# Optimization experiments

Hardware: AMD Instinct MI355X
Metric: run time of the kernel (lower is better)

## Reference

```python
import jax, jax.numpy as jnp
import numpy as np

EPS = 1e-05


def _project_to_poincare_ball(v, eps=EPS):
    # scale = clamp((1-eps)/(||v||+1e-10), max=1.0)
    norm = jnp.sqrt(jnp.sum(v * v, axis=-1, keepdims=True))
    scale = jnp.minimum((1.0 - eps) / (norm + 1e-10), 1.0)
    return v * scale


def setup_inputs() -> dict:
    key = jax.random.key(0)
    k1, k2 = jax.random.split(key)
    B, S, D, V = 2, 2048, 1024, 32000
    hidden_states = jax.random.normal(k1, (B, S, D), dtype=jnp.float32)
    weight = jax.random.normal(k2, (V, D), dtype=jnp.float32)
    return {"hidden_states": hidden_states, "weight": weight}


def reference(hidden_states, weight):
    eps = EPS
    B, S, D = hidden_states.shape
    x = _project_to_poincare_ball(hidden_states.reshape(-1, D), eps)  # (N, D)
    y = _project_to_poincare_ball(weight, eps)                        # (V, D)

    x_sq = jnp.sum(x * x, axis=-1)  # (N,)
    y_sq = jnp.sum(y * y, axis=-1)  # (V,)

    # NOTE: the original feeds this (non-squared) distance into the Poincare
    # formula (variable misnamed diff_norm_sq); we reproduce that exactly.
    d2 = x_sq[:, None] + y_sq[None, :] - 2.0 * jnp.einsum('nd,vd->nv', x, y)
    dist_euclid = jnp.sqrt(jnp.maximum(d2, 0.0))  # (N, V)

    denom = (1.0 - x_sq)[:, None] * (1.0 - y_sq)[None, :]  # (N, V)
    argument = 1.0 + 2.0 * dist_euclid / (denom + eps)
    argument = jnp.maximum(argument, 1.0 + eps)
    distances = jnp.arccosh(argument)  # (N, V)

    logits = -distances
    return logits.reshape(B, S, -1)
```

## Files before the change

### kernel.cpp

```cpp
#include <hip/hip_runtime.h>
#include <math.h>
#include <stdint.h>

#define EPS 1e-5f

typedef __bf16 bf16x8 __attribute__((ext_vector_type(8)));
typedef __bf16 bf16x4 __attribute__((ext_vector_type(4)));
typedef float  f32x4  __attribute__((ext_vector_type(4)));

constexpr int D  = 1024;

__global__ __launch_bounds__(256) void project_convert_kernel(
    const float* __restrict__ src, __bf16* __restrict__ dst,
    float* __restrict__ q_out)
{
    const int row = blockIdx.x;
    const int t = threadIdx.x;
    const float4 v = *(const float4*)(src + (size_t)row * D + t * 4);
    float s = v.x * v.x + v.y * v.y + v.z * v.z + v.w * v.w;
#pragma unroll
    for (int off = 32; off > 0; off >>= 1) s += __shfl_down(s, off);
    __shared__ float partial[4];
    __shared__ float s_scale;
    if ((t & 63) == 0) partial[t >> 6] = s;
    __syncthreads();
    if (t == 0) {
        float tot = partial[0] + partial[1] + partial[2] + partial[3];
        float norm = sqrtf(tot);
        float sc = fminf((1.0f - EPS) / (norm + 1e-10f), 1.0f);
        s_scale = sc;
        q_out[row] = sc * sc * tot;
    }
    __syncthreads();
    const float sc = s_scale;
    bf16x4 o = { (__bf16)(v.x * sc), (__bf16)(v.y * sc),
                 (__bf16)(v.z * sc), (__bf16)(v.w * sc) };
    *(bf16x4*)(dst + (size_t)row * D + t * 4) = o;
}

__device__ __forceinline__ void gload16(const void* g, void* l)
{
    __builtin_amdgcn_global_load_lds(
        (const __attribute__((address_space(1))) uint32_t*)g,
        (__attribute__((address_space(3))) uint32_t*)l, 16, 0, 0);
}

#define WAITVM(N) asm volatile("s_waitcnt vmcnt(" #N ")" ::: "memory")
#define WAITLGKM0 asm volatile("s_waitcnt lgkmcnt(0)" ::: "memory")

__global__ __launch_bounds__(512, 2) void hyp_gemm_256_kernel(
    const __bf16* __restrict__ Xb, const __bf16* __restrict__ Yb,
    const float* __restrict__ xq, const float* __restrict__ yq,
    float* __restrict__ out, int V, int nbx)
{
    constexpr int BK = 64;
    constexpr int KT = D / BK;
    constexpr int BUFB = 256 * BK * 2;

    __shared__ __bf16 As[2 * 256 * BK];
    __shared__ __bf16 Bs[2 * 256 * BK];

    const int wg = blockIdx.x;
    const int c = (gridDim.x & 7) ? wg : ((wg & 7) * (gridDim.x >> 3) + (wg >> 3));
    const int m0 = (c / nbx) * 256;
    const int n0 = (c % nbx) * 256;

    const int t = threadIdx.x;

    const int rt = t >> 3;
    const int gsrc = (t & 7) ^ (rt & 7);
    const char* xg = (const char*)(Xb + (size_t)(m0 + rt) * D) + gsrc * 16;
    const char* yg = (const char*)(Yb + (size_t)(n0 + rt) * D) + gsrc * 16;

    const int lane = t & 63;
    const int ln   = lane & 15;
    const int quad = lane >> 4;
    const int wave = t >> 6;
    const int wm = (wave >> 2) * 128;
    const int wn = (wave & 3) * 64;
    const int swz = ln & 7;

    f32x4 acc[8][4] = {};

    auto STAGE = [&](int kt, int b) {
        const int ko = kt * 128;
#pragma unroll
        for (int j = 0; j < 4; ++j)
            gload16(xg + j * 131072 + ko, (char*)As + b * BUFB + j * 8192 + t * 16);
#pragma unroll
        for (int j = 0; j < 4; ++j)
            gload16(yg + j * 131072 + ko, (char*)Bs + b * BUFB + j * 8192 + t * 16);
    };

    auto COMPUTE = [&](int b) {
        const char* Ab = (const char*)As + b * BUFB;
        const char* Bb = (const char*)Bs + b * BUFB;
#pragma unroll
        for (int ks = 0; ks < 2; ++ks) {
            const int ga = ((ks * 4 + quad) ^ swz) * 16;
            bf16x8 af[8], bfr[4];
#pragma unroll
            for (int i = 0; i < 8; ++i)
                af[i] = *(const bf16x8*)(Ab + (wm + i * 16 + ln) * 128 + ga);
#pragma unroll
            for (int i = 0; i < 4; ++i)
                bfr[i] = *(const bf16x8*)(Bb + (wn + i * 16 + ln) * 128 + ga);
            __builtin_amdgcn_s_setprio(1);
#pragma unroll
            for (int mt = 0; mt < 8; ++mt)
#pragma unroll
                for (int nt = 0; nt < 4; ++nt)
                    acc[mt][nt] = __builtin_amdgcn_mfma_f32_16x16x32_bf16(
                        af[mt], bfr[nt], acc[mt][nt], 0, 0, 0);
            __builtin_amdgcn_s_setprio(0);
        }
    };

    STAGE(0, 0);
#pragma unroll 2
    for (int kt = 0; kt < KT; ++kt) {
        const int b = kt & 1;
        if (kt + 1 < KT) {
            STAGE(kt + 1, b ^ 1);
            WAITVM(8);
        } else {
            WAITVM(0);
        }
        __builtin_amdgcn_sched_barrier(0);
        __builtin_amdgcn_s_barrier();
        __builtin_amdgcn_sched_barrier(0);
        COMPUTE(b);
        WAITLGKM0;
        __builtin_amdgcn_sched_barrier(0);
        __builtin_amdgcn_s_barrier();
        __builtin_amdgcn_sched_barrier(0);
    }

    float yqv[4], omy[4];
    int gcv[4];
#pragma unroll
    for (int nt = 0; nt < 4; ++nt) {
        const int gc = n0 + wn + nt * 16 + ln;
        gcv[nt] = gc;
        yqv[nt] = yq[gc];
        omy[nt] = 1.0f - yqv[nt];
    }
#pragma unroll
    for (int mt = 0; mt < 8; ++mt) {
#pragma unroll
        for (int r = 0; r < 4; ++r) {
            const int gm = m0 + wm + mt * 16 + quad * 4 + r;
            const float xqv = xq[gm];
            const float omx = 1.0f - xqv;
            float* orow = out + (size_t)gm * V;
#pragma unroll
            for (int nt = 0; nt < 4; ++nt) {
                const float dot = acc[mt][nt][r];
                float d2 = fmaxf(xqv + yqv[nt] - 2.0f * dot, 0.0f);
                float d  = __builtin_amdgcn_sqrtf(d2);
                float denom = omx * omy[nt] + EPS;
                float w = d * __builtin_amdgcn_rcpf(denom);
                float res;
                if (__builtin_expect(w >= 4.0f, 1)) {
                    res = __logf(2.0f + 4.0f * w);
                } else {
                    float arg = fmaxf(1.0f + 2.0f * w, 1.0f + EPS);
                    res = __logf(arg + __builtin_amdgcn_sqrtf(arg * arg - 1.0f));
                }
                orow[gcv[nt]] = -res;
            }
        }
    }
}

constexpr int FBM = 128, FBN = 128;
constexpr int LDT = 40;

__global__ __launch_bounds__(256) void row_stats_kernel(
    const float* __restrict__ src, float* __restrict__ scale_out,
    float* __restrict__ sq_out)
{
    const int row = blockIdx.x;
    const int t = threadIdx.x;
    const float4 v = *(const float4*)(src + (size_t)row * D + t * 4);
    float s = v.x * v.x + v.y * v.y + v.z * v.z + v.w * v.w;
#pragma unroll
    for (int off = 32; off > 0; off >>= 1) s += __shfl_down(s, off);
    __shared__ float partial[4];
    if ((t & 63) == 0) partial[t >> 6] = s;
    __syncthreads();
    if (t == 0) {
        float tot = partial[0] + partial[1] + partial[2] + partial[3];
        float norm = sqrtf(tot);
        float sc = fminf((1.0f - EPS) / (norm + 1e-10f), 1.0f);
        scale_out[row] = sc;
        sq_out[row] = sc * sc * tot;
    }
}

__global__ __launch_bounds__(256) void hyp_gemm_kernel(
    const float* __restrict__ X, const float* __restrict__ Y,
    const float* __restrict__ sx, const float* __restrict__ xq,
    const float* __restrict__ sy, const float* __restrict__ yq,
    float* __restrict__ out, int V)
{
    constexpr int BK = 32;
    __shared__ __bf16 As[FBM * LDT];
    __shared__ __bf16 Bs[FBN * LDT];

    const int t  = threadIdx.x;
    const int m0 = blockIdx.y * FBM;
    const int n0 = blockIdx.x * FBN;

    const int sr = t >> 3;
    const int scol = t & 7;

    const float* xg = X + (size_t)(m0 + sr) * D + scol * 4;
    const float* yg = Y + (size_t)(n0 + sr) * D + scol * 4;

    const int lane = t & 63;
    const int wave = t >> 6;
    const int wm = (wave & 1) * 64;
    const int wn = (wave >> 1) * 64;
    const int ln = lane & 15;
    const int quad = lane >> 4;

    f32x4 acc[4][4] = {};

    float4 pa[4], pb[4];
#pragma unroll
    for (int j = 0; j < 4; ++j) {
        pa[j] = *(const float4*)(xg + (size_t)j * 32 * D);
        pb[j] = *(const float4*)(yg + (size_t)j * 32 * D);
    }

    constexpr int KT = D / BK;
    for (int kt = 0; kt < KT; ++kt) {
        __syncthreads();
#pragma unroll
        for (int j = 0; j < 4; ++j) {
            bf16x4 a4 = { (__bf16)pa[j].x, (__bf16)pa[j].y, (__bf16)pa[j].z, (__bf16)pa[j].w };
            bf16x4 b4 = { (__bf16)pb[j].x, (__bf16)pb[j].y, (__bf16)pb[j].z, (__bf16)pb[j].w };
            *(bf16x4*)&As[(sr + 32 * j) * LDT + scol * 4] = a4;
            *(bf16x4*)&Bs[(sr + 32 * j) * LDT + scol * 4] = b4;
        }
        __syncthreads();
        if (kt + 1 < KT) {
            const int koff = (kt + 1) * BK;
#pragma unroll
            for (int j = 0; j < 4; ++j) {
                pa[j] = *(const float4*)(xg + (size_t)j * 32 * D + koff);
                pb[j] = *(const float4*)(yg + (size_t)j * 32 * D + koff);
            }
        }
        bf16x8 af[4], bfr[4];
#pragma unroll
        for (int i = 0; i < 4; ++i) {
            af[i]  = *(const bf16x8*)&As[(wm + i * 16 + ln) * LDT + quad * 8];
            bfr[i] = *(const bf16x8*)&Bs[(wn + i * 16 + ln) * LDT + quad * 8];
        }
#pragma unroll
        for (int mt = 0; mt < 4; ++mt)
#pragma unroll
            for (int nt = 0; nt < 4; ++nt)
                acc[mt][nt] = __builtin_amdgcn_mfma_f32_16x16x32_bf16(
                    af[mt], bfr[nt], acc[mt][nt], 0, 0, 0);
    }

    float yqv[4], syv[4];
    int gcv[4];
#pragma unroll
    for (int nt = 0; nt < 4; ++nt) {
        const int gc = n0 + wn + nt * 16 + ln;
        gcv[nt] = gc;
        yqv[nt] = yq[gc];
        syv[nt] = sy[gc];
    }
#pragma unroll
    for (int mt = 0; mt < 4; ++mt) {
#pragma unroll
        for (int r = 0; r < 4; ++r) {
            const int gm = m0 + wm + mt * 16 + quad * 4 + r;
            const float xqv = xq[gm];
            const float sxv = sx[gm];
            const float omx = 1.0f - xqv;
            float* orow = out + (size_t)gm * V;
#pragma unroll
            for (int nt = 0; nt < 4; ++nt) {
                const float raw = acc[mt][nt][r];
                const float dot = sxv * syv[nt] * raw;
                float d2 = xqv + yqv[nt] - 2.0f * dot;
                float dd = __builtin_amdgcn_sqrtf(fmaxf(d2, 0.0f));
                float denom = omx * (1.0f - yqv[nt]) + EPS;
                float arg = 1.0f + 2.0f * dd * __builtin_amdgcn_rcpf(denom);
                arg = fmaxf(arg, 1.0f + EPS);
                float res = -__logf(arg + __builtin_amdgcn_sqrtf(arg * arg - 1.0f));
                orow[gcv[nt]] = res;
            }
        }
    }
}

extern "C" void kernel_launch(void* const* d_in, const int* in_sizes, int n_in,
                              void* d_out, int out_size, void* d_ws, size_t ws_size,
                              hipStream_t stream)
{
    const float* X = (const float*)d_in[0];
    const float* Y = (const float*)d_in[1];
    float* out = (float*)d_out;

    const int N = in_sizes[0] / D;
    const int V = in_sizes[1] / D;

    const size_t need = (size_t)(N + V) * D * 2 + (size_t)(N + V) * 4;

    if (ws_size >= need && (N % 256) == 0 && (V % 256) == 0) {
        __bf16* Xb = (__bf16*)d_ws;
        __bf16* Yb = Xb + (size_t)N * D;
        float* xq = (float*)(Yb + (size_t)V * D);
        float* yq = xq + N;

        project_convert_kernel<<<N, 256, 0, stream>>>(X, Xb, xq);
        project_convert_kernel<<<V, 256, 0, stream>>>(Y, Yb, yq);

        const int nbx = V / 256;
        const int nwg = nbx * (N / 256);
        hyp_gemm_256_kernel<<<nwg, 512, 0, stream>>>(Xb, Yb, xq, yq, out, V, nbx);
    } else {
        float* sx = (float*)d_ws;
        float* xq = sx + N;
        float* sy = xq + N;
        float* yq = sy + V;

        row_stats_kernel<<<N, 256, 0, stream>>>(X, sx, xq);
        row_stats_kernel<<<V, 256, 0, stream>>>(Y, sy, yq);

        dim3 grid(V / FBN, N / FBM);
        hyp_gemm_kernel<<<grid, 256, 0, stream>>>(X, Y, sx, xq, sy, yq, out, V);
    }
}
```

Before: 909.2 us.

## Switch GEMM main loop to 4-stage BK=32 LDS ring with one barrier

Halves the K tile to 32 and uses a four-buffer LDS ring with prefetch distance two, so each iteration needs only one workgroup barrier instead of two and no explicit LDS-read wait. The XOR swizzle is reworked for the 64-byte row pitch. The goal is to overlap global-to-LDS loads with MFMA work and cut barrier stalls. In exchange there are twice as many loop iterations, smaller MFMA bursts per barrier, and possible LDS bank conflicts from the narrower swizzle.

```diff
diff --git a/kernel.cpp b/kernel.cpp
--- a/kernel.cpp
+++ b/kernel.cpp
@@ -46,19 +46,18 @@
 }
 
 #define WAITVM(N) asm volatile("s_waitcnt vmcnt(" #N ")" ::: "memory")
-#define WAITLGKM0 asm volatile("s_waitcnt lgkmcnt(0)" ::: "memory")
 
 __global__ __launch_bounds__(512, 2) void hyp_gemm_256_kernel(
     const __bf16* __restrict__ Xb, const __bf16* __restrict__ Yb,
     const float* __restrict__ xq, const float* __restrict__ yq,
     float* __restrict__ out, int V, int nbx)
 {
-    constexpr int BK = 64;
-    constexpr int KT = D / BK;
+    constexpr int BK   = 32;
+    constexpr int KT   = D / BK;
     constexpr int BUFB = 256 * BK * 2;
 
-    __shared__ __bf16 As[2 * 256 * BK];
-    __shared__ __bf16 Bs[2 * 256 * BK];
+    __shared__ __bf16 As[4 * 256 * BK];
+    __shared__ __bf16 Bs[4 * 256 * BK];
 
     const int wg = blockIdx.x;
     const int c = (gridDim.x & 7) ? wg : ((wg & 7) * (gridDim.x >> 3) + (wg >> 3));
@@ -67,8 +66,8 @@
 
     const int t = threadIdx.x;
 
-    const int rt = t >> 3;
-    const int gsrc = (t & 7) ^ (rt & 7);
+    const int rt   = t >> 2;
+    const int gsrc = (t & 3) ^ ((t >> 3) & 3);
     const char* xg = (const char*)(Xb + (size_t)(m0 + rt) * D) + gsrc * 16;
     const char* yg = (const char*)(Yb + (size_t)(n0 + rt) * D) + gsrc * 16;
 
@@ -78,63 +77,60 @@
     const int wave = t >> 6;
     const int wm = (wave >> 2) * 128;
     const int wn = (wave & 3) * 64;
-    const int swz = ln & 7;
+    const int ga = (quad ^ ((ln >> 1) & 3)) * 16;
 
     f32x4 acc[8][4] = {};
 
     auto STAGE = [&](int kt, int b) {
-        const int ko = kt * 128;
-#pragma unroll
-        for (int j = 0; j < 4; ++j)
-            gload16(xg + j * 131072 + ko, (char*)As + b * BUFB + j * 8192 + t * 16);
-#pragma unroll
-        for (int j = 0; j < 4; ++j)
-            gload16(yg + j * 131072 + ko, (char*)Bs + b * BUFB + j * 8192 + t * 16);
+        const int ko = kt * 64;
+        gload16(xg + ko,          (char*)As + b * BUFB + t * 16);
+        gload16(xg + ko + 262144, (char*)As + b * BUFB + 8192 + t * 16);
+        gload16(yg + ko,          (char*)Bs + b * BUFB + t * 16);
+        gload16(yg + ko + 262144, (char*)Bs + b * BUFB + 8192 + t * 16);
     };
 
     auto COMPUTE = [&](int b) {
         const char* Ab = (const char*)As + b * BUFB;
         const char* Bb = (const char*)Bs + b * BUFB;
-#pragma unroll
-        for (int ks = 0; ks < 2; ++ks) {
-            const int ga = ((ks * 4 + quad) ^ swz) * 16;
-            bf16x8 af[8], bfr[4];
-#pragma unroll
-            for (int i = 0; i < 8; ++i)
-                af[i] = *(const bf16x8*)(Ab + (wm + i * 16 + ln) * 128 + ga);
-#pragma unroll
-            for (int i = 0; i < 4; ++i)
-                bfr[i] = *(const bf16x8*)(Bb + (wn + i * 16 + ln) * 128 + ga);
-            __builtin_amdgcn_s_setprio(1);
-#pragma unroll
-            for (int mt = 0; mt < 8; ++mt)
-#pragma unroll
-                for (int nt = 0; nt < 4; ++nt)
-                    acc[mt][nt] = __builtin_amdgcn_mfma_f32_16x16x32_bf16(
-                        af[mt], bfr[nt], acc[mt][nt], 0, 0, 0);
-            __builtin_amdgcn_s_setprio(0);
-        }
+        bf16x8 af[8], bfr[4];
+#pragma unroll
+        for (int i = 0; i < 8; ++i)
+            af[i] = *(const bf16x8*)(Ab + (wm + i * 16 + ln) * 64 + ga);
+#pragma unroll
+        for (int i = 0; i < 4; ++i)
+            bfr[i] = *(const bf16x8*)(Bb + (wn + i * 16 + ln) * 64 + ga);
+        __builtin_amdgcn_s_setprio(1);
+#pragma unroll
+        for (int mt = 0; mt < 8; ++mt)
+#pragma unroll
+            for (int nt = 0; nt < 4; ++nt)
+                acc[mt][nt] = __builtin_amdgcn_mfma_f32_16x16x32_bf16(
+                    af[mt], bfr[nt], acc[mt][nt], 0, 0, 0);
+        __builtin_amdgcn_s_setprio(0);
     };
 
     STAGE(0, 0);
-#pragma unroll 2
-    for (int kt = 0; kt < KT; ++kt) {
-        const int b = kt & 1;
-        if (kt + 1 < KT) {
-            STAGE(kt + 1, b ^ 1);
-            WAITVM(8);
-        } else {
-            WAITVM(0);
-        }
+    STAGE(1, 1);
+
+#pragma unroll
+    for (int kt = 0; kt < KT - 2; ++kt) {
+        STAGE(kt + 2, (kt + 2) & 3);
         __builtin_amdgcn_sched_barrier(0);
+        WAITVM(8);
         __builtin_amdgcn_s_barrier();
         __builtin_amdgcn_sched_barrier(0);
-        COMPUTE(b);
-        WAITLGKM0;
-        __builtin_amdgcn_sched_barrier(0);
-        __builtin_amdgcn_s_barrier();
-        __builtin_amdgcn_sched_barrier(0);
-    }
+        COMPUTE(kt & 3);
+    }
+    __builtin_amdgcn_sched_barrier(0);
+    WAITVM(4);
+    __builtin_amdgcn_s_barrier();
+    __builtin_amdgcn_sched_barrier(0);
+    COMPUTE((KT - 2) & 3);
+    __builtin_amdgcn_sched_barrier(0);
+    WAITVM(0);
+    __builtin_amdgcn_s_barrier();
+    __builtin_amdgcn_sched_barrier(0);
+    COMPUTE((KT - 1) & 3);
 
     float yqv[4], omy[4];
     int gcv[4];
```

After: 899.4 us. About the same (-1.1%).

## Split GEMM mainloop into half-tile stages interleaved with MFMA quadrants

Applied to the files above, without the earlier changes.

Restructures the bf16 GEMM main loop so the 256x64 A/B tiles are staged as separate 128-row halves. Global-to-LDS loads for the next iterations are spread between four MFMA quadrant phases, with extra barriers, instead of one bulk prefetch per iteration. The aim is finer overlap of memory traffic with matrix compute, in the style of HipKittens 8-wave ping-pong schedules. It also drops the XCD-aware block remapping and adds many more s_barrier calls, which may add sync overhead or hurt L2 locality.

```diff
diff --git a/kernel.cpp b/kernel.cpp
--- a/kernel.cpp
+++ b/kernel.cpp
@@ -45,95 +45,156 @@
         (__attribute__((address_space(3))) uint32_t*)l, 16, 0, 0);
 }
 
-#define WAITVM(N) asm volatile("s_waitcnt vmcnt(" #N ")" ::: "memory")
-#define WAITLGKM0 asm volatile("s_waitcnt lgkmcnt(0)" ::: "memory")
+#define WAITVM(N)  asm volatile("s_waitcnt vmcnt(" #N ")" ::: "memory")
+#define WAITLGKM0  asm volatile("s_waitcnt lgkmcnt(0)" ::: "memory")
+#define SBAR()     __builtin_amdgcn_s_barrier()
+#define SCHED0()   __builtin_amdgcn_sched_barrier(0)
 
 __global__ __launch_bounds__(512, 2) void hyp_gemm_256_kernel(
     const __bf16* __restrict__ Xb, const __bf16* __restrict__ Yb,
     const float* __restrict__ xq, const float* __restrict__ yq,
     float* __restrict__ out, int V, int nbx)
 {
-    constexpr int BK = 64;
-    constexpr int KT = D / BK;
-    constexpr int BUFB = 256 * BK * 2;
-
-    __shared__ __bf16 As[2 * 256 * BK];
-    __shared__ __bf16 Bs[2 * 256 * BK];
-
-    const int wg = blockIdx.x;
-    const int c = (gridDim.x & 7) ? wg : ((wg & 7) * (gridDim.x >> 3) + (wg >> 3));
+    constexpr int KT   = D / 64;
+    constexpr int HALF = 16384;
+
+    __shared__ char As[4 * HALF];
+    __shared__ char Bs[4 * HALF];
+
+    const int c  = blockIdx.x;
     const int m0 = (c / nbx) * 256;
     const int n0 = (c % nbx) * 256;
 
     const int t = threadIdx.x;
 
-    const int rt = t >> 3;
-    const int gsrc = (t & 7) ^ (rt & 7);
-    const char* xg = (const char*)(Xb + (size_t)(m0 + rt) * D) + gsrc * 16;
-    const char* yg = (const char*)(Yb + (size_t)(n0 + rt) * D) + gsrc * 16;
+    const int rt   = t >> 3;
+    const int gsrc = ((t & 7) ^ (rt & 7)) * 16;
+    const char* xrow = (const char*)Xb + (size_t)(m0 + rt) * 2048 + gsrc;
+    const char* yrow = (const char*)Yb + (size_t)(n0 + rt) * 2048 + gsrc;
+
+    auto STAGE_A = [&](int k, int h) {
+        char* dst = As + ((k & 1) * 2 + h) * HALF + t * 16;
+        const char* src = xrow + (size_t)(h * 128) * 2048 + k * 128;
+        gload16(src, dst);
+        gload16(src + 64 * 2048, dst + 8192);
+    };
+    auto STAGE_B = [&](int k, int h) {
+        char* dst = Bs + ((k & 1) * 2 + h) * HALF + t * 16;
+        const char* src = yrow + (size_t)(h * 128) * 2048 + k * 128;
+        gload16(src, dst);
+        gload16(src + 64 * 2048, dst + 8192);
+    };
 
     const int lane = t & 63;
     const int ln   = lane & 15;
     const int quad = lane >> 4;
     const int wave = t >> 6;
-    const int wm = (wave >> 2) * 128;
-    const int wn = (wave & 3) * 64;
-    const int swz = ln & 7;
+    const int ha   = wave >> 2;
+    const int hb   = (wave & 3) >> 1;
+    const int brow = (wave & 1) * 64;
+    const int wm   = ha * 128;
+    const int wn   = (wave & 3) * 64;
+    const int swz  = ln & 7;
+
+    const int ga0 = ((0 * 4 + quad) ^ swz) * 16;
+    const int ga1 = ((1 * 4 + quad) ^ swz) * 16;
 
     f32x4 acc[8][4] = {};
-
-    auto STAGE = [&](int kt, int b) {
-        const int ko = kt * 128;
-#pragma unroll
-        for (int j = 0; j < 4; ++j)
-            gload16(xg + j * 131072 + ko, (char*)As + b * BUFB + j * 8192 + t * 16);
-#pragma unroll
-        for (int j = 0; j < 4; ++j)
-            gload16(yg + j * 131072 + ko, (char*)Bs + b * BUFB + j * 8192 + t * 16);
-    };
-
-    auto COMPUTE = [&](int b) {
-        const char* Ab = (const char*)As + b * BUFB;
-        const char* Bb = (const char*)Bs + b * BUFB;
-#pragma unroll
-        for (int ks = 0; ks < 2; ++ks) {
-            const int ga = ((ks * 4 + quad) ^ swz) * 16;
-            bf16x8 af[8], bfr[4];
-#pragma unroll
-            for (int i = 0; i < 8; ++i)
-                af[i] = *(const bf16x8*)(Ab + (wm + i * 16 + ln) * 128 + ga);
-#pragma unroll
-            for (int i = 0; i < 4; ++i)
-                bfr[i] = *(const bf16x8*)(Bb + (wn + i * 16 + ln) * 128 + ga);
-            __builtin_amdgcn_s_setprio(1);
-#pragma unroll
-            for (int mt = 0; mt < 8; ++mt)
-#pragma unroll
-                for (int nt = 0; nt < 4; ++nt)
-                    acc[mt][nt] = __builtin_amdgcn_mfma_f32_16x16x32_bf16(
-                        af[mt], bfr[nt], acc[mt][nt], 0, 0, 0);
-            __builtin_amdgcn_s_setprio(0);
-        }
-    };
-
-    STAGE(0, 0);
+    bf16x8 a03[8], a47[8], b[8];
+
+    auto LDA03 = [&](const char* sa) {
+#pragma unroll
+        for (int i = 0; i < 4; ++i) {
+            const char* r = sa + (i * 16 + ln) * 128;
+            a03[i * 2 + 0] = *(const bf16x8*)(r + ga0);
+            a03[i * 2 + 1] = *(const bf16x8*)(r + ga1);
+        }
+    };
+    auto LDA47 = [&](const char* sa) {
+#pragma unroll
+        for (int i = 0; i < 4; ++i) {
+            const char* r = sa + ((i + 4) * 16 + ln) * 128;
+            a47[i * 2 + 0] = *(const bf16x8*)(r + ga0);
+            a47[i * 2 + 1] = *(const bf16x8*)(r + ga1);
+        }
+    };
+    auto LDB = [&](const char* sb) {
+#pragma unroll
+        for (int i = 0; i < 4; ++i) {
+            const char* r = sb + (brow + i * 16 + ln) * 128;
+            b[i * 2 + 0] = *(const bf16x8*)(r + ga0);
+            b[i * 2 + 1] = *(const bf16x8*)(r + ga1);
+        }
+    };
+    auto MM = [&](bf16x8* a, int mBase, int nBase) {
+        __builtin_amdgcn_s_setprio(1);
+#pragma unroll
+        for (int mi = 0; mi < 4; ++mi)
+#pragma unroll
+            for (int ni = 0; ni < 2; ++ni)
+#pragma unroll
+                for (int ks = 0; ks < 2; ++ks)
+                    acc[mBase + mi][nBase + ni] =
+                        __builtin_amdgcn_mfma_f32_16x16x32_bf16(
+                            a[mi * 2 + ks], b[(nBase + ni) * 2 + ks],
+                            acc[mBase + mi][nBase + ni], 0, 0, 0);
+        __builtin_amdgcn_s_setprio(0);
+    };
+
+    STAGE_A(0, 0); STAGE_A(0, 1); STAGE_B(0, 0); STAGE_B(0, 1);
+    STAGE_B(1, 0); STAGE_A(1, 0); STAGE_A(1, 1);
+
 #pragma unroll 2
-    for (int kt = 0; kt < KT; ++kt) {
-        const int b = kt & 1;
-        if (kt + 1 < KT) {
-            STAGE(kt + 1, b ^ 1);
-            WAITVM(8);
-        } else {
-            WAITVM(0);
-        }
-        __builtin_amdgcn_sched_barrier(0);
-        __builtin_amdgcn_s_barrier();
-        __builtin_amdgcn_sched_barrier(0);
-        COMPUTE(b);
-        WAITLGKM0;
-        __builtin_amdgcn_sched_barrier(0);
-        __builtin_amdgcn_s_barrier();
-        __builtin_amdgcn_sched_barrier(0);
+    for (int kt = 0; kt < KT - 2; ++kt) {
+        const char* sa = As + ((kt & 1) * 2 + ha) * HALF;
+        const char* sb = Bs + ((kt & 1) * 2 + hb) * HALF;
+        WAITVM(6); SCHED0(); SBAR(); SCHED0();
+        LDA03(sa); LDB(sb);
+        STAGE_B(kt + 1, 1);
+        SBAR(); WAITLGKM0; SCHED0();
+        MM(a03, 0, 0);
+        SBAR();
+        LDA47(sa);
+        STAGE_B(kt + 2, 0);
+        SBAR(); WAITLGKM0; SCHED0();
+        MM(a03, 0, 2);
+        SBAR();
+        STAGE_A(kt + 2, 0);
+        SBAR();
+        MM(a47, 4, 2);
+        SBAR();
+        STAGE_A(kt + 2, 1);
+        SBAR();
+        MM(a47, 4, 0);
+        SBAR();
+    }
+    {
+        const char* sa = As + (0 * 2 + ha) * HALF;
+        const char* sb = Bs + (0 * 2 + hb) * HALF;
+        WAITVM(6); SCHED0(); SBAR(); SCHED0();
+        LDA03(sa); LDB(sb);
+        STAGE_B(KT - 1, 1);
+        SBAR(); WAITLGKM0; SCHED0();
+        MM(a03, 0, 0);
+        SBAR();
+        LDA47(sa);
+        SBAR(); WAITLGKM0; SCHED0();
+        MM(a03, 0, 2);
+        MM(a47, 4, 2);
+        MM(a47, 4, 0);
+    }
+    {
+        const char* sa = As + (1 * 2 + ha) * HALF;
+        const char* sb = Bs + (1 * 2 + hb) * HALF;
+        WAITVM(0); SCHED0(); SBAR(); SCHED0();
+        LDA03(sa); LDB(sb);
+        WAITLGKM0; SCHED0();
+        MM(a03, 0, 0);
+        MM(a03, 0, 2);
+        LDA47(sa);
+        WAITLGKM0; SCHED0();
+        MM(a47, 4, 2);
+        MM(a47, 4, 0);
     }
 
     float yqv[4], omy[4];
```

Measured after the change: 897.5 us. About the same (-1.3%).
